# Performance work log

Measured on AMD Instinct MI355X. Metric: run time of the kernel, lower is better.

Reference implementation:

```python
import jax, jax.numpy as jnp
import numpy as np

N_NODES = 100000
N_EDGES = 3200000
N_FEAT = 16
N_LAYERS = 4


def setup_inputs() -> dict:
    key = jax.random.key(0)
    k1, k2, k3, k4 = jax.random.split(key, 4)
    h_0 = jax.random.normal(k1, (N_NODES, N_FEAT), dtype=jnp.float32)
    edge_index = jax.random.randint(k2, (2, N_EDGES), 0, N_NODES, dtype=jnp.int64)
    weight_tensor = jax.random.normal(k3, (N_EDGES,), dtype=jnp.float32)
    # per-layer learned per-edge weights, init normal(std=1/sqrt(E)) as in torch
    layer_weights = jax.random.normal(k4, (N_LAYERS, N_EDGES), dtype=jnp.float32) / np.sqrt(N_EDGES)
    return {"h_0": h_0, "edge_index": edge_index, "weight_tensor": weight_tensor,
            "layer_weights": layer_weights}


def _layer(h, src, dst, edge_scale):
    # gather x_j = h[src]  [E, F], scale by per-edge scalar, scatter-add to dst
    msg = edge_scale[:, None] * h[src]
    return jax.ops.segment_sum(msg, dst, num_segments=N_NODES)


def reference(h_0, edge_index, weight_tensor, layer_weights):
    # PyG default flow source_to_target: x_j = x[edge_index[0]], aggregate at edge_index[1]
    src = edge_index[0]
    dst = edge_index[1]
    h = h_0
    for k in range(N_LAYERS - 1):
        h = _layer(h, src, dst, weight_tensor * layer_weights[k])
        h = h + h_0
    h = _layer(h, src, dst, weight_tensor * layer_weights[N_LAYERS - 1])
    return jax.nn.sigmoid(2.0 * h)
```

## Files before the change

### kernel.cpp

```cpp
#include <hip/hip_runtime.h>
#include <hip/hip_fp16.h>

#define NNODES   100000
#define NFEAT    16
#define NEDGES   3200000
#define EH       1600000
#define NB       250
#define NODES_PB 400
#define NCH      125
#define CHK      12800
#define CAP      7168
#define N8       (NNODES * 8)

__global__ __launch_bounds__(1024) void hist_chunk(
    const int* __restrict__ dst, int ebase, int* __restrict__ cnt )
{
    __shared__ int h[NB];
    int c = blockIdx.x;
    for (int i = threadIdx.x; i < NB; i += 1024) h[i] = 0;
    __syncthreads();
    int base = ebase + c * CHK;
    for (int i = threadIdx.x; i < CHK; i += 1024) {
        int d = dst[base + i];
        atomicAdd(&h[d / NODES_PB], 1);
    }
    __syncthreads();
    for (int i = threadIdx.x; i < NB; i += 1024) cnt[c * NB + i] = h[i];
}

__global__ __launch_bounds__(256) void scan_chunks(
    int* __restrict__ cnt, int* __restrict__ tot)
{
    __shared__ int x[256];
    int b = blockIdx.x, t = threadIdx.x;
    int v = (t < NCH) ? cnt[t * NB + b] : 0;
    x[t] = v;
    __syncthreads();
    for (int off = 1; off < 256; off <<= 1) {
        int y = (t >= off) ? x[t - off] : 0;
        __syncthreads();
        x[t] += y;
        __syncthreads();
    }
    if (t < NCH) cnt[t * NB + b] = x[t] - v;
    if (t == NCH - 1) tot[b] = x[t];
}

__global__ __launch_bounds__(256) void scan_tot(
    const int* __restrict__ tot, int* __restrict__ bb)
{
    __shared__ int x[256];
    int t = threadIdx.x;
    int v = (t < NB) ? tot[t] : 0;
    x[t] = v;
    __syncthreads();
    for (int off = 1; off < 256; off <<= 1) {
        int y = (t >= off) ? x[t - off] : 0;
        __syncthreads();
        x[t] += y;
        __syncthreads();
    }
    if (t < NB) bb[t] = x[t] - v;
    if (t == NB - 1) bb[NB] = x[t];
}

__global__ __launch_bounds__(1024) void scatter_bins(
    const int*   __restrict__ src,
    const int*   __restrict__ dst,
    const float* __restrict__ wt,
    const float* __restrict__ lw,
    int ebase,
    const int*   __restrict__ cnt,
    const int*   __restrict__ bb,
    unsigned int* __restrict__ binsE)
{
    __shared__ int cur[NB];
    int c = blockIdx.x;
    for (int i = threadIdx.x; i < NB; i += 1024)
        cur[i] = bb[i] + cnt[c * NB + i];
    __syncthreads();
    int base = ebase + c * CHK;
    for (int i = threadIdx.x; i < CHK; i += 1024) {
        int e = base + i;
        int d = dst[e];
        int b  = d / NODES_PB;
        int dl = d - b * NODES_PB;
        float w = wt[e];
        __half2 w01 = __floats2half2_rn(w * lw[e],              w * lw[NEDGES + e]);
        __half2 w23 = __floats2half2_rn(w * lw[2 * NEDGES + e], w * lw[3 * NEDGES + e]);
        int slot = atomicAdd(&cur[b], 1);
        unsigned int* p = binsE + 3u * (unsigned int)slot;
        p[0] = (unsigned int)src[e] | ((unsigned int)dl << 17);
        p[1] = *(const unsigned int*)&w01;
        p[2] = *(const unsigned int*)&w23;
    }
}

__global__ __launch_bounds__(512) void bucket_csr(
    const int*          __restrict__ bb,
    const unsigned int* __restrict__ binsE,
    unsigned int*       __restrict__ csrA,
    unsigned short*     __restrict__ w0,
    unsigned short*     __restrict__ w1,
    unsigned short*     __restrict__ w2,
    unsigned short*     __restrict__ w3,
    int*                __restrict__ offs)
{
    __shared__ unsigned int   regA[CAP];
    __shared__ unsigned int   regC[CAP];
    __shared__ unsigned short pi[CAP];
    __shared__ int hist[NODES_PB];
    __shared__ int cur[NODES_PB];
    __shared__ int sc[512];
    int b  = blockIdx.x, t = threadIdx.x;
    int e0 = bb[b];
    int cnt = bb[b + 1] - e0;
    if (cnt > CAP) cnt = CAP;

    for (int i = t; i < NODES_PB; i += 512) hist[i] = 0;
    __syncthreads();
    for (int i = t; i < cnt; i += 512) {
        unsigned int a = binsE[3u * (unsigned int)(e0 + i)];
        regA[i] = a;
        atomicAdd(&hist[a >> 17], 1);
    }
    __syncthreads();
    int v = (t < NODES_PB) ? hist[t] : 0;
    sc[t] = v;
    __syncthreads();
    for (int off = 1; off < 512; off <<= 1) {
        int y = (t >= off) ? sc[t - off] : 0;
        __syncthreads();
        sc[t] += y;
        __syncthreads();
    }
    if (t < NODES_PB) {
        int excl = sc[t] - v;
        cur[t] = excl;
        offs[b * NODES_PB + t] = e0 + excl;
    }
    if (b == 0 && t == 0) offs[NNODES] = EH;
    __syncthreads();
    unsigned short* inv = (unsigned short*)regC;
    for (int i = t; i < cnt; i += 512) {
        unsigned int a = regA[i];
        int slot = atomicAdd(&cur[a >> 17], 1);
        pi[i]  = (unsigned short)slot;
        inv[slot] = (unsigned short)i;
    }
    __syncthreads();
    for (int s = t; s < cnt; s += 512) {
        csrA[e0 + s] = regA[inv[s]] & 0x1FFFFu;
    }
    __syncthreads();
    unsigned short* wA0 = (unsigned short*)regA;
    unsigned short* wA1 = wA0 + CAP;
    unsigned short* wC2 = (unsigned short*)regC;
    unsigned short* wC3 = wC2 + CAP;
    for (int i = t; i < cnt; i += 512) {
        unsigned int u01 = binsE[3u * (unsigned int)(e0 + i) + 1];
        unsigned int u23 = binsE[3u * (unsigned int)(e0 + i) + 2];
        int s = pi[i];
        wA0[s] = (unsigned short)(u01 & 0xFFFFu);
        wA1[s] = (unsigned short)(u01 >> 16);
        wC2[s] = (unsigned short)(u23 & 0xFFFFu);
        wC3[s] = (unsigned short)(u23 >> 16);
    }
    __syncthreads();
    for (int s = t; s < cnt; s += 512) {
        w0[e0 + s] = wA0[s];
        w1[e0 + s] = wA1[s];
        w2[e0 + s] = wC2[s];
        w3[e0 + s] = wC3[s];
    }
}

__global__ __launch_bounds__(256) void conv16(
    const float2* __restrict__ in, __half2* __restrict__ out, int n2)
{
    int i = blockIdx.x * 256 + threadIdx.x;
    if (i < n2) {
        float2 v = in[i];
        out[i] = __floats2half2_rn(v.x, v.y);
    }
}

__global__ __launch_bounds__(256) void pullq(
    const int*            __restrict__ offs1,
    const int*            __restrict__ offs2,
    const unsigned int*   __restrict__ csrA1,
    const unsigned int*   __restrict__ csrA2,
    const unsigned short* __restrict__ wk1,
    const unsigned short* __restrict__ wk2,
    const __half2*        __restrict__ h16,
    __half2*              __restrict__ partial)
{
    int t = blockIdx.x * 256 + threadIdx.x;
    int n = t >> 5;
    if (n >= NNODES) return;
    int grp = (t >> 3) & 3;
    int f2  = t & 7;

    int j01 = offs1[n], e1 = offs1[n + 1];
    int j02 = offs2[n], e2 = offs2[n + 1];
    int m1 = (j01 + e1) >> 1;
    int m2 = (j02 + e2) >> 1;

    const unsigned int*   A;
    const unsigned short* W;
    int js, je;
    if (grp < 2) {
        A = csrA1; W = wk1;
        js = (grp == 0) ? j01 : m1;
        je = (grp == 0) ? m1  : e1;
    } else {
        A = csrA2; W = wk2;
        js = (grp == 2) ? j02 : m2;
        je = (grp == 2) ? m2  : e2;
    }

    float ax = 0.f, ay = 0.f;
    int j = js;
    for (; j + 3 < je; j += 4) {
        unsigned int s0 = A[j],     s1 = A[j + 1];
        unsigned int s2 = A[j + 2], s3 = A[j + 3];
        float w0 = __half2float(__ushort_as_half(W[j]));
        float w1 = __half2float(__ushort_as_half(W[j + 1]));
        float w2 = __half2float(__ushort_as_half(W[j + 2]));
        float w3 = __half2float(__ushort_as_half(W[j + 3]));
        float2 v0 = __half22float2(h16[s0 * 8 + f2]);
        float2 v1 = __half22float2(h16[s1 * 8 + f2]);
        float2 v2 = __half22float2(h16[s2 * 8 + f2]);
        float2 v3 = __half22float2(h16[s3 * 8 + f2]);
        ax = fmaf(w0, v0.x, ax); ay = fmaf(w0, v0.y, ay);
        ax = fmaf(w1, v1.x, ax); ay = fmaf(w1, v1.y, ay);
        ax = fmaf(w2, v2.x, ax); ay = fmaf(w2, v2.y, ay);
        ax = fmaf(w3, v3.x, ax); ay = fmaf(w3, v3.y, ay);
    }
    for (; j < je; ++j) {
        unsigned int s = A[j];
        float w = __half2float(__ushort_as_half(W[j]));
        float2 v = __half22float2(h16[s * 8 + f2]);
        ax = fmaf(w, v.x, ax); ay = fmaf(w, v.y, ay);
    }

    partial[grp * N8 + n * 8 + f2] = __floats2half2_rn(ax, ay);
}

template<bool SIG>
__global__ __launch_bounds__(256) void combine(
    const __half2* __restrict__ partial,
    const float2*  __restrict__ h0,
    void*          __restrict__ hout)
{
    int i = blockIdx.x * 256 + threadIdx.x;
    if (i >= N8) return;
    float2 p0 = __half22float2(partial[0 * N8 + i]);
    float2 p1 = __half22float2(partial[1 * N8 + i]);
    float2 p2 = __half22float2(partial[2 * N8 + i]);
    float2 p3 = __half22float2(partial[3 * N8 + i]);
    float sx = (p0.x + p1.x) + (p2.x + p3.x);
    float sy = (p0.y + p1.y) + (p2.y + p3.y);
    if (SIG) {
        float2 r;
        r.x = 1.f / (1.f + expf(-2.f * sx));
        r.y = 1.f / (1.f + expf(-2.f * sy));
        ((float2*)hout)[i] = r;
    } else {
        float2 b = h0[i];
        ((__half2*)hout)[i] = __floats2half2_rn(sx + b.x, sy + b.y);
    }
}

__global__ __launch_bounds__(256) void scatter_layer(
    const int* __restrict__ src, const int* __restrict__ dst,
    const float* __restrict__ wt, const float* __restrict__ lw,
    const float* __restrict__ h, float* __restrict__ acc)
{
    long t = (long)blockIdx.x * blockDim.x + threadIdx.x;
    int e = (int)(t >> 4);
    if (e >= NEDGES) return;
    int f = (int)(t & 15);
    float w = wt[e] * lw[e];
    atomicAdd(&acc[dst[e] * NFEAT + f], w * h[src[e] * NFEAT + f]);
}
__global__ __launch_bounds__(256) void sigmoid_inplace(float* __restrict__ out, int n)
{
    int i = blockIdx.x * blockDim.x + threadIdx.x;
    if (i < n) out[i] = 1.f / (1.f + expf(-2.f * out[i]));
}

extern "C" void kernel_launch(void* const* d_in, const int* in_sizes, int n_in,
                              void* d_out, int out_size, void* d_ws, size_t ws_size,
                              hipStream_t stream)
{
    const float* h0 = (const float*)d_in[0];
    const int*   ei = (const int*)d_in[1];
    const float* wt = (const float*)d_in[2];
    const float* lw = (const float*)d_in[3];

    const int* src = ei;
    const int* dst = ei + NEDGES;

    const size_t off_cnt   = 0;
    const size_t off_tot   = 125056;
    const size_t off_bb    = 126080;
    const size_t off_offs1 = 127104;
    const size_t off_offs2 = off_offs1 + 400128;
    const size_t off_csrA  = off_offs2 + 400128;
    const size_t off_w     = off_csrA + (size_t)2 * EH * 4;
    const size_t off_bins  = off_w + (size_t)8 * EH * 2;
    const size_t need      = off_bins + (size_t)3 * EH * 4;

    if (ws_size < need) {
        const size_t hbytes = (size_t)NNODES * NFEAT * sizeof(float);
        float* hw = (float*)d_ws;
        float* ho = (float*)d_out;
        dim3 blk(256), grd(((long)NEDGES * 16 + 255) / 256);
        hipMemcpyAsync(hw, h0, hbytes, hipMemcpyDeviceToDevice, stream);
        scatter_layer<<<grd, blk, 0, stream>>>(src, dst, wt, lw + 0L * NEDGES, h0, hw);
        hipMemcpyAsync(ho, h0, hbytes, hipMemcpyDeviceToDevice, stream);
        scatter_layer<<<grd, blk, 0, stream>>>(src, dst, wt, lw + 1L * NEDGES, hw, ho);
        hipMemcpyAsync(hw, h0, hbytes, hipMemcpyDeviceToDevice, stream);
        scatter_layer<<<grd, blk, 0, stream>>>(src, dst, wt, lw + 2L * NEDGES, ho, hw);
        hipMemsetAsync(ho, 0, hbytes, stream);
        scatter_layer<<<grd, blk, 0, stream>>>(src, dst, wt, lw + 3L * NEDGES, hw, ho);
        int n = NNODES * NFEAT;
        sigmoid_inplace<<<(n + 255) / 256, 256, 0, stream>>>(ho, n);
        return;
    }

    char* ws = (char*)d_ws;
    int*            cnt   = (int*)(ws + off_cnt);
    int*            tot   = (int*)(ws + off_tot);
    int*            bb    = (int*)(ws + off_bb);
    int*            offs1 = (int*)(ws + off_offs1);
    int*            offs2 = (int*)(ws + off_offs2);
    unsigned int*   csrA1 = (unsigned int*)(ws + off_csrA);
    unsigned int*   csrA2 = csrA1 + EH;
    unsigned short* wbase = (unsigned short*)(ws + off_w);
    unsigned short* w0_1 = wbase + 0L * EH; unsigned short* w1_1 = wbase + 1L * EH;
    unsigned short* w2_1 = wbase + 2L * EH; unsigned short* w3_1 = wbase + 3L * EH;
    unsigned short* w0_2 = wbase + 4L * EH; unsigned short* w1_2 = wbase + 5L * EH;
    unsigned short* w2_2 = wbase + 6L * EH; unsigned short* w3_2 = wbase + 7L * EH;
    unsigned int*   binsE = (unsigned int*)(ws + off_bins);
    const size_t HB = (size_t)NNODES * NFEAT * 2;
    __half2* hb0      = (__half2*)(ws + off_bins);
    __half2* partials = (__half2*)(ws + off_bins + HB);
    __half2* hbA      = (__half2*)(ws + off_bins + 5 * HB);
    __half2* hbB      = (__half2*)d_out;
    float*   hout     = (float*)d_out;

    hist_chunk  <<<NCH, 1024, 0, stream>>>(dst, 0, cnt);
    scan_chunks <<<NB,   256, 0, stream>>>(cnt, tot);
    scan_tot    <<<1,    256, 0, stream>>>(tot, bb);
    scatter_bins<<<NCH, 1024, 0, stream>>>(src, dst, wt, lw, 0, cnt, bb, binsE);
    bucket_csr  <<<NB,   512, 0, stream>>>(bb, binsE, csrA1, w0_1, w1_1, w2_1, w3_1, offs1);
    hist_chunk  <<<NCH, 1024, 0, stream>>>(dst, EH, cnt);
    scan_chunks <<<NB,   256, 0, stream>>>(cnt, tot);
    scan_tot    <<<1,    256, 0, stream>>>(tot, bb);
    scatter_bins<<<NCH, 1024, 0, stream>>>(src, dst, wt, lw, EH, cnt, bb, binsE);
    bucket_csr  <<<NB,   512, 0, stream>>>(bb, binsE, csrA2, w0_2, w1_2, w2_2, w3_2, offs2);

    conv16<<<(N8 + 255) / 256, 256, 0, stream>>>((const float2*)h0, hb0, N8);

    dim3 blk(256), grdP((NNODES * 32) / 256), grdC((N8 + 255) / 256);
    const float2* h0f2 = (const float2*)h0;
    pullq<<<grdP, blk, 0, stream>>>(offs1, offs2, csrA1, csrA2, w0_1, w0_2, hb0, partials);
    combine<false><<<grdC, blk, 0, stream>>>(partials, h0f2, hbA);
    pullq<<<grdP, blk, 0, stream>>>(offs1, offs2, csrA1, csrA2, w1_1, w1_2, hbA, partials);
    combine<false><<<grdC, blk, 0, stream>>>(partials, h0f2, hbB);
    pullq<<<grdP, blk, 0, stream>>>(offs1, offs2, csrA1, csrA2, w2_1, w2_2, hbB, partials);
    combine<false><<<grdC, blk, 0, stream>>>(partials, h0f2, hbA);
    pullq<<<grdP, blk, 0, stream>>>(offs1, offs2, csrA1, csrA2, w3_1, w3_2, hbA, partials);
    combine<true ><<<grdC, blk, 0, stream>>>(partials, h0f2, hout);
}
```

Measured before the change: 256.0 us.

## Fuse partial combine into pull kernel via wave shuffles; use smaller binning chunks

```diff
diff --git a/kernel.cpp b/kernel.cpp
--- a/kernel.cpp
+++ b/kernel.cpp
@@ -7,36 +7,36 @@
 #define EH       1600000
 #define NB       250
 #define NODES_PB 400
-#define NCH      125
-#define CHK      12800
+#define NCH      500
+#define CHK      3200
 #define CAP      7168
 #define N8       (NNODES * 8)
 
-__global__ __launch_bounds__(1024) void hist_chunk(
+__global__ __launch_bounds__(256) void hist_chunk(
     const int* __restrict__ dst, int ebase, int* __restrict__ cnt )
 {
     __shared__ int h[NB];
     int c = blockIdx.x;
-    for (int i = threadIdx.x; i < NB; i += 1024) h[i] = 0;
+    for (int i = threadIdx.x; i < NB; i += 256) h[i] = 0;
     __syncthreads();
     int base = ebase + c * CHK;
-    for (int i = threadIdx.x; i < CHK; i += 1024) {
+    for (int i = threadIdx.x; i < CHK; i += 256) {
         int d = dst[base + i];
         atomicAdd(&h[d / NODES_PB], 1);
     }
     __syncthreads();
-    for (int i = threadIdx.x; i < NB; i += 1024) cnt[c * NB + i] = h[i];
-}
-
-__global__ __launch_bounds__(256) void scan_chunks(
+    for (int i = threadIdx.x; i < NB; i += 256) cnt[c * NB + i] = h[i];
+}
+
+__global__ __launch_bounds__(512) void scan_chunks(
     int* __restrict__ cnt, int* __restrict__ tot)
 {
-    __shared__ int x[256];
+    __shared__ int x[512];
     int b = blockIdx.x, t = threadIdx.x;
     int v = (t < NCH) ? cnt[t * NB + b] : 0;
     x[t] = v;
     __syncthreads();
-    for (int off = 1; off < 256; off <<= 1) {
+    for (int off = 1; off < 512; off <<= 1) {
         int y = (t >= off) ? x[t - off] : 0;
         __syncthreads();
         x[t] += y;
@@ -64,7 +64,7 @@
     if (t == NB - 1) bb[NB] = x[t];
 }
 
-__global__ __launch_bounds__(1024) void scatter_bins(
+__global__ __launch_bounds__(256) void scatter_bins(
     const int*   __restrict__ src,
     const int*   __restrict__ dst,
     const float* __restrict__ wt,
@@ -76,11 +76,11 @@
 {
     __shared__ int cur[NB];
     int c = blockIdx.x;
-    for (int i = threadIdx.x; i < NB; i += 1024)
+    for (int i = threadIdx.x; i < NB; i += 256)
         cur[i] = bb[i] + cnt[c * NB + i];
     __syncthreads();
     int base = ebase + c * CHK;
-    for (int i = threadIdx.x; i < CHK; i += 1024) {
+    for (int i = threadIdx.x; i < CHK; i += 256) {
         int e = base + i;
         int d = dst[e];
         int b  = d / NODES_PB;
@@ -185,7 +185,8 @@
     }
 }
 
-__global__ __launch_bounds__(256) void pullq(
+template<bool SIG>
+__global__ __launch_bounds__(256) void pullr(
     const int*            __restrict__ offs1,
     const int*            __restrict__ offs2,
     const unsigned int*   __restrict__ csrA1,
@@ -193,7 +194,8 @@
     const unsigned short* __restrict__ wk1,
     const unsigned short* __restrict__ wk2,
     const __half2*        __restrict__ h16,
-    __half2*              __restrict__ partial)
+    const float2*         __restrict__ h0,
+    void*                 __restrict__ hout)
 {
     int t = blockIdx.x * 256 + threadIdx.x;
     int n = t >> 5;
@@ -244,31 +246,20 @@
         ax = fmaf(w, v.x, ax); ay = fmaf(w, v.y, ay);
     }
 
-    partial[grp * N8 + n * 8 + f2] = __floats2half2_rn(ax, ay);
-}
-
-template<bool SIG>
-__global__ __launch_bounds__(256) void combine(
-    const __half2* __restrict__ partial,
-    const float2*  __restrict__ h0,
-    void*          __restrict__ hout)
-{
-    int i = blockIdx.x * 256 + threadIdx.x;
-    if (i >= N8) return;
-    float2 p0 = __half22float2(partial[0 * N8 + i]);
-    float2 p1 = __half22float2(partial[1 * N8 + i]);
-    float2 p2 = __half22float2(partial[2 * N8 + i]);
-    float2 p3 = __half22float2(partial[3 * N8 + i]);
-    float sx = (p0.x + p1.x) + (p2.x + p3.x);
-    float sy = (p0.y + p1.y) + (p2.y + p3.y);
-    if (SIG) {
-        float2 r;
-        r.x = 1.f / (1.f + expf(-2.f * sx));
-        r.y = 1.f / (1.f + expf(-2.f * sy));
-        ((float2*)hout)[i] = r;
-    } else {
-        float2 b = h0[i];
-        ((__half2*)hout)[i] = __floats2half2_rn(sx + b.x, sy + b.y);
+    ax += __shfl_xor(ax, 8);  ay += __shfl_xor(ay, 8);
+    ax += __shfl_xor(ax, 16); ay += __shfl_xor(ay, 16);
+
+    if (grp == 0) {
+        int o = n * 8 + f2;
+        if (SIG) {
+            float2 r;
+            r.x = 1.f / (1.f + expf(-2.f * ax));
+            r.y = 1.f / (1.f + expf(-2.f * ay));
+            ((float2*)hout)[o] = r;
+        } else {
+            float2 b = h0[o];
+            ((__half2*)hout)[o] = __floats2half2_rn(ax + b.x, ay + b.y);
+        }
     }
 }
 
@@ -303,9 +294,9 @@
     const int* dst = ei + NEDGES;
 
     const size_t off_cnt   = 0;
-    const size_t off_tot   = 125056;
-    const size_t off_bb    = 126080;
-    const size_t off_offs1 = 127104;
+    const size_t off_tot   = 500224;
+    const size_t off_bb    = 501248;
+    const size_t off_offs1 = 502272;
     const size_t off_offs2 = off_offs1 + 400128;
     const size_t off_csrA  = off_offs2 + 400128;
     const size_t off_w     = off_csrA + (size_t)2 * EH * 4;
@@ -345,33 +336,28 @@
     unsigned short* w2_2 = wbase + 6L * EH; unsigned short* w3_2 = wbase + 7L * EH;
     unsigned int*   binsE = (unsigned int*)(ws + off_bins);
     const size_t HB = (size_t)NNODES * NFEAT * 2;
-    __half2* hb0      = (__half2*)(ws + off_bins);
-    __half2* partials = (__half2*)(ws + off_bins + HB);
-    __half2* hbA      = (__half2*)(ws + off_bins + 5 * HB);
-    __half2* hbB      = (__half2*)d_out;
-    float*   hout     = (float*)d_out;
-
-    hist_chunk  <<<NCH, 1024, 0, stream>>>(dst, 0, cnt);
-    scan_chunks <<<NB,   256, 0, stream>>>(cnt, tot);
-    scan_tot    <<<1,    256, 0, stream>>>(tot, bb);
-    scatter_bins<<<NCH, 1024, 0, stream>>>(src, dst, wt, lw, 0, cnt, bb, binsE);
-    bucket_csr  <<<NB,   512, 0, stream>>>(bb, binsE, csrA1, w0_1, w1_1, w2_1, w3_1, offs1);
-    hist_chunk  <<<NCH, 1024, 0, stream>>>(dst, EH, cnt);
-    scan_chunks <<<NB,   256, 0, stream>>>(cnt, tot);
-    scan_tot    <<<1,    256, 0, stream>>>(tot, bb);
-    scatter_bins<<<NCH, 1024, 0, stream>>>(src, dst, wt, lw, EH, cnt, bb, binsE);
-    bucket_csr  <<<NB,   512, 0, stream>>>(bb, binsE, csrA2, w0_2, w1_2, w2_2, w3_2, offs2);
+    __half2* hb0  = (__half2*)(ws + off_bins);
+    __half2* hbA  = (__half2*)(ws + off_bins + HB);
+    __half2* hbB  = (__half2*)d_out;
+    float*   hout = (float*)d_out;
+
+    hist_chunk  <<<NCH, 256, 0, stream>>>(dst, 0, cnt);
+    scan_chunks <<<NB,  512, 0, stream>>>(cnt, tot);
+    scan_tot    <<<1,   256, 0, stream>>>(tot, bb);
+    scatter_bins<<<NCH, 256, 0, stream>>>(src, dst, wt, lw, 0, cnt, bb, binsE);
+    bucket_csr  <<<NB,  512, 0, stream>>>(bb, binsE, csrA1, w0_1, w1_1, w2_1, w3_1, offs1);
+    hist_chunk  <<<NCH, 256, 0, stream>>>(dst, EH, cnt);
+    scan_chunks <<<NB,  512, 0, stream>>>(cnt, tot);
+    scan_tot    <<<1,   256, 0, stream>>>(tot, bb);
+    scatter_bins<<<NCH, 256, 0, stream>>>(src, dst, wt, lw, EH, cnt, bb, binsE);
+    bucket_csr  <<<NB,  512, 0, stream>>>(bb, binsE, csrA2, w0_2, w1_2, w2_2, w3_2, offs2);
 
     conv16<<<(N8 + 255) / 256, 256, 0, stream>>>((const float2*)h0, hb0, N8);
 
-    dim3 blk(256), grdP((NNODES * 32) / 256), grdC((N8 + 255) / 256);
+    dim3 blk(256), grdP((NNODES * 32) / 256);
     const float2* h0f2 = (const float2*)h0;
-    pullq<<<grdP, blk, 0, stream>>>(offs1, offs2, csrA1, csrA2, w0_1, w0_2, hb0, partials);
-    combine<false><<<grdC, blk, 0, stream>>>(partials, h0f2, hbA);
-    pullq<<<grdP, blk, 0, stream>>>(offs1, offs2, csrA1, csrA2, w1_1, w1_2, hbA, partials);
-    combine<false><<<grdC, blk, 0, stream>>>(partials, h0f2, hbB);
-    pullq<<<grdP, blk, 0, stream>>>(offs1, offs2, csrA1, csrA2, w2_1, w2_2, hbB, partials);
-    combine<false><<<grdC, blk, 0, stream>>>(partials, h0f2, hbA);
-    pullq<<<grdP, blk, 0, stream>>>(offs1, offs2, csrA1, csrA2, w3_1, w3_2, hbA, partials);
-    combine<true ><<<grdC, blk, 0, stream>>>(partials, h0f2, hout);
-}
+    pullr<false><<<grdP, blk, 0, stream>>>(offs1, offs2, csrA1, csrA2, w0_1, w0_2, hb0, h0f2, hbA);
+    pullr<false><<<grdP, blk, 0, stream>>>(offs1, offs2, csrA1, csrA2, w1_1, w1_2, hbA, h0f2, hbB);
+    pullr<false><<<grdP, blk, 0, stream>>>(offs1, offs2, csrA1, csrA2, w2_1, w2_2, hbB, h0f2, hbA);
+    pullr<true ><<<grdP, blk, 0, stream>>>(offs1, offs2, csrA1, csrA2, w3_1, w3_2, hbA, h0f2, hout);
+}
```

Measured after the change: 245.2 us. 1.04x faster.
